# Kernel tuning notes

Measured on AMD Instinct MI355X. Metric: run time of the kernel, lower is better.

The kernel has to match this reference:

```python
import jax, jax.numpy as jnp
import numpy as np

EMB = 1024
HEADS = 16
B, N = 2, 2048

def setup_inputs() -> dict:
    key = jax.random.key(0)
    ks = jax.random.split(key, 9)
    s = 1.0 / np.sqrt(EMB)
    return {
        "x": jax.random.normal(ks[0], (B, N, EMB), dtype=jnp.float32),
        "Wq": jax.random.normal(ks[1], (EMB, EMB), dtype=jnp.float32) * s,
        "bq": jax.random.normal(ks[2], (EMB,), dtype=jnp.float32) * 0.01,
        "Wk": jax.random.normal(ks[3], (EMB, EMB), dtype=jnp.float32) * s,
        "bk": jax.random.normal(ks[4], (EMB,), dtype=jnp.float32) * 0.01,
        "Wv": jax.random.normal(ks[5], (EMB, EMB), dtype=jnp.float32) * s,
        "bv": jax.random.normal(ks[6], (EMB,), dtype=jnp.float32) * 0.01,
        "Wo": jax.random.normal(ks[7], (EMB, EMB), dtype=jnp.float32) * s,
        "bo": jax.random.normal(ks[8], (EMB,), dtype=jnp.float32) * 0.01,
    }

def _split_heads(t):
    b, n, e = t.shape
    return t.reshape(b, n, HEADS, e // HEADS).transpose(0, 2, 1, 3)  # b h n d

def reference(x, Wq, bq, Wk, bk, Wv, bv, Wo, bo):
    q = _split_heads(x @ Wq + bq)
    k = _split_heads(x @ Wk + bk)
    v = _split_heads(x @ Wv + bv)
    # NOTE: original scales by sqrt(emb_size), not sqrt(head_dim)
    scaling = jnp.asarray(EMB, x.dtype) ** 0.5
    energy = jnp.einsum('bhqd,bhkd->bhqk', q, k)
    att = jax.nn.softmax(energy / scaling, axis=-1)
    out = jnp.einsum('bhqk,bhkd->bhqd', att, v)
    out = out.transpose(0, 2, 1, 3).reshape(x.shape[0], x.shape[1], EMB)
    return out @ Wo + bo
```

## Files before the change

kernel.cpp:

```cpp
#include <hip/hip_runtime.h>
#include <hip/hip_bf16.h>

typedef __bf16 bf16_t;
typedef bf16_t bf16x8 __attribute__((ext_vector_type(8)));
typedef float f32x4 __attribute__((ext_vector_type(4)));
typedef float f32x2 __attribute__((ext_vector_type(2)));
typedef float f32x16 __attribute__((ext_vector_type(16)));

#define EMB 1024
#define HEADS 16
#define BATCH 2
#define SEQ 2048
#define HD 64
#define TOKENS (BATCH * SEQ)

__device__ __forceinline__ void gld16(bf16_t* lds_dst, const bf16_t* g_src) {
    __builtin_amdgcn_global_load_lds(
        (const __attribute__((address_space(1))) unsigned int*)g_src,
        (__attribute__((address_space(3))) unsigned int*)lds_dst, 16, 0, 0);
}

__device__ __forceinline__ unsigned cvt_pk_bf16(float lo, float hi) {
    unsigned r;
    asm("v_cvt_pk_bf16_f32 %0, %1, %2" : "=v"(r) : "v"(lo), "v"(hi));
    return r;
}

__device__ __forceinline__ float exp2_fast(float x) {
#if __has_builtin(__builtin_amdgcn_exp2f)
    return __builtin_amdgcn_exp2f(x);
#else
    return __expf(x * 0.69314718056f);
#endif
}

#define WAITV(N) asm volatile("s_waitcnt vmcnt(" #N ")" ::: "memory")
#define BAR() __builtin_amdgcn_s_barrier()

__global__ __launch_bounds__(256) void prep_all(
    const float* __restrict__ x, bf16_t* __restrict__ xb,
    const float* __restrict__ W0, const float* __restrict__ W1,
    const float* __restrict__ W2, const float* __restrict__ W3,
    bf16_t* __restrict__ T0, bf16_t* __restrict__ T1,
    bf16_t* __restrict__ T2, bf16_t* __restrict__ T3) {
    __shared__ __align__(16) bf16_t T[64][72];
    if (blockIdx.x < 1024) {
        size_t i = ((size_t)blockIdx.x * 256 + threadIdx.x) * 16;
        f32x4 v0 = *(const f32x4*)&x[i];
        f32x4 v1 = *(const f32x4*)&x[i + 4];
        f32x4 v2 = *(const f32x4*)&x[i + 8];
        f32x4 v3 = *(const f32x4*)&x[i + 12];
        bf16x8 o0, o1;
#pragma unroll
        for (int j = 0; j < 4; ++j) {
            o0[j] = (bf16_t)v0[j]; o0[4 + j] = (bf16_t)v1[j];
            o1[j] = (bf16_t)v2[j]; o1[4 + j] = (bf16_t)v3[j];
        }
        *(bf16x8*)&xb[i] = o0;
        *(bf16x8*)&xb[i + 8] = o1;
        return;
    }
    int t = blockIdx.x - 1024;
    int z = t >> 8, rid = t & 255;
    const float* src = (z == 0) ? W0 : (z == 1) ? W1 : (z == 2) ? W2 : W3;
    bf16_t* dst = (z == 0) ? T0 : (z == 1) ? T1 : (z == 2) ? T2 : T3;
    int k0 = (rid >> 4) * 64, n0 = (rid & 15) * 64;
    int r = threadIdx.x >> 2, c4 = (threadIdx.x & 3) * 16;
    f32x4 v[4];
#pragma unroll
    for (int q = 0; q < 4; ++q)
        v[q] = *(const f32x4*)&src[(size_t)(k0 + r) * 1024 + n0 + c4 + q * 4];
#pragma unroll
    for (int j = 0; j < 16; ++j) T[c4 + j][r] = (bf16_t)v[j >> 2][j & 3];
    __syncthreads();
    bf16x8 o0 = *(const bf16x8*)&T[r][c4];
    bf16x8 o1 = *(const bf16x8*)&T[r][c4 + 8];
    *(bf16x8*)&dst[(size_t)(n0 + r) * 1024 + k0 + c4] = o0;
    *(bf16x8*)&dst[(size_t)(n0 + r) * 1024 + k0 + c4 + 8] = o1;
}

template <typename TO>
__global__ __launch_bounds__(512) void gemm256(
    const bf16_t* __restrict__ A, const bf16_t* __restrict__ W,
    const float* __restrict__ b0, const float* __restrict__ b1, const float* __restrict__ b2,
    TO* __restrict__ o0, TO* __restrict__ o1, TO* __restrict__ o2,
    int md0, int md1, int md2, float sc0, float sc1, float sc2,
    int MP, int CM, int CSH, int NP) {
    __shared__ __align__(16) bf16_t As[3][256 * 64];
    __shared__ __align__(16) bf16_t Bs[3][128 * 64];

    const int tid = threadIdx.x, w = tid >> 6, lane = tid & 63;
    const int quad = lane >> 4, c = lane & 15;
    const int wm = (w >> 1) * 64, wn = (w & 1) * 64;

    const int lin = blockIdx.x;
    const int xc = lin & 7, t = lin >> 3;
    const int mi = MP * (xc & CM) + (t % MP);
    const int ni = NP * (xc >> CSH) + (t / MP);
    const int m0 = mi * 256, n0 = ni * 128;

    const int z = n0 >> 10;
    const float* bias = (z == 0) ? b0 : (z == 1) ? b1 : b2;
    TO* out = (z == 0) ? o0 : (z == 1) ? o1 : o2;
    const int mode = (z == 0) ? md0 : (z == 1) ? md1 : md2;
    const float scale = (z == 0) ? sc0 : (z == 1) ? sc1 : sc2;
    const int nz = n0 & 1023;

    f32x4 acc[4][4];
#pragma unroll
    for (int i = 0; i < 4; ++i)
#pragma unroll
        for (int j = 0; j < 4; ++j) acc[i][j] = (f32x4){0.f, 0.f, 0.f, 0.f};

    const int r8 = lane >> 3, sg = lane & 7;
    const int g8 = (sg ^ r8) * 8;
    const bf16_t* Ag = A + (size_t)m0 * 1024;
    const bf16_t* Bg = W + (size_t)n0 * 1024;
    int gA[4], lA[4], gB[2], lB[2];
#pragma unroll
    for (int s = 0; s < 4; ++s) {
        lA[s] = (w * 32 + s * 8) * 64;
        gA[s] = (w * 32 + s * 8 + r8) * 1024 + g8;
    }
#pragma unroll
    for (int s = 0; s < 2; ++s) {
        lB[s] = (w * 16 + s * 8) * 64;
        gB[s] = (w * 16 + s * 8 + r8) * 1024 + g8;
    }

    const int so = (quad ^ (c & 7)) * 8;
    int rA[4], rB[4];
#pragma unroll
    for (int i = 0; i < 4; ++i) {
        rA[i] = (wm + i * 16 + c) * 64;
        rB[i] = (wn + i * 16 + c) * 64;
    }

#define STAGE(BUF, T)                                                          \
    {                                                                          \
        int kn = (T) * 64;                                                     \
        _Pragma("unroll")                                                      \
        for (int s = 0; s < 4; ++s) gld16(&As[BUF][lA[s]], &Ag[gA[s] + kn]);   \
        _Pragma("unroll")                                                      \
        for (int s = 0; s < 2; ++s) gld16(&Bs[BUF][lB[s]], &Bg[gB[s] + kn]);   \
    }

#define FRAGS(CUR)                                                             \
    {                                                                          \
        _Pragma("unroll")                                                      \
        for (int ks = 0; ks < 2; ++ks) {                                       \
            int sk = so ^ (ks << 5);                                           \
            bf16x8 af[4], bfv[4];                                              \
            _Pragma("unroll")                                                  \
            for (int i = 0; i < 4; ++i)                                        \
                af[i] = *(const bf16x8*)&As[CUR][rA[i] + sk];                  \
            _Pragma("unroll")                                                  \
            for (int i = 0; i < 4; ++i)                                        \
                bfv[i] = *(const bf16x8*)&Bs[CUR][rB[i] + sk];                 \
            __builtin_amdgcn_s_setprio(1);                                     \
            _Pragma("unroll")                                                  \
            for (int mt = 0; mt < 4; ++mt)                                     \
                _Pragma("unroll")                                              \
                for (int nt = 0; nt < 4; ++nt)                                 \
                    acc[mt][nt] = __builtin_amdgcn_mfma_f32_16x16x32_bf16(     \
                        af[mt], bfv[nt], acc[mt][nt], 0, 0, 0);                \
            __builtin_amdgcn_s_setprio(0);                                     \
        }                                                                      \
    }

#define GSTEP(T, CUR)                                                          \
    {                                                                          \
        WAITV(6);                                                              \
        BAR();                                                                 \
        STAGE(((CUR) + 2) % 3, (T) + 2)                                        \
        FRAGS(CUR)                                                             \
    }

    STAGE(0, 0)
    STAGE(1, 1)
    for (int T = 0; T < 12; T += 3) {
        GSTEP(T, 0)
        GSTEP(T + 1, 1)
        GSTEP(T + 2, 2)
    }
    GSTEP(12, 0)
    GSTEP(13, 1)
    WAITV(6); BAR(); FRAGS(2)
    WAITV(0); BAR(); FRAGS(0)
#undef GSTEP
#undef FRAGS
#undef STAGE

    typedef TO TOx4 __attribute__((ext_vector_type(4)));
#pragma unroll
    for (int nt = 0; nt < 4; ++nt) {
        int colz = nz + wn + nt * 16 + c;
        float bv = bias[colz];
#pragma unroll
        for (int mt = 0; mt < 4; ++mt) {
            if (mode == 2) {
                int row = m0 + wm + mt * 16 + quad * 4;
                int bb = row >> 11, n = row & 2047;
                int hh = colz >> 6, d = colz & 63;
                TOx4 pk;
#pragma unroll
                for (int r = 0; r < 4; ++r)
                    pk[r] = (TO)((acc[mt][nt][r] + bv) * scale);
                *(TOx4*)&out[((size_t)(bb * HEADS + hh) * HD + d) * SEQ + n] = pk;
            } else {
#pragma unroll
                for (int r = 0; r < 4; ++r) {
                    int row = m0 + wm + mt * 16 + quad * 4 + r;
                    float v = (acc[mt][nt][r] + bv) * scale;
                    size_t idx;
                    if (mode == 0) {
                        idx = (size_t)row * 1024 + colz;
                    } else {
                        int bb = row >> 11, n = row & 2047;
                        int hh = colz >> 6, d = colz & 63;
                        idx = ((size_t)(bb * HEADS + hh) * SEQ + n) * HD + d;
                    }
                    out[idx] = (TO)v;
                }
            }
        }
    }
}

__global__ __launch_bounds__(256, 2) void attn_kernel(
    const bf16_t* __restrict__ Q, const bf16_t* __restrict__ K,
    const bf16_t* __restrict__ Vt, bf16_t* __restrict__ O) {
    __shared__ __align__(16) bf16_t Ks[2][2 * 64 * 64];
    __shared__ __align__(16) bf16_t Vs[2][2 * 64 * 64];

    const int tid = threadIdx.x, w = tid >> 6, lane = tid & 63;
    const int hi = lane >> 5, lq = lane & 31;

    const int lin = blockIdx.x + (blockIdx.y << 4);
    const int xcd = lin & 7, slot = lin >> 3;
    const int bh = xcd + ((slot >> 4) << 3);
    const int q0 = (slot & 15) << 7;
    const int b = bh >> 4, h = bh & 15;

    const int srow8 = lane >> 3, sch = lane & 7;

    const bf16_t* Kg0 = K + (size_t)bh * SEQ * HD;
    const bf16_t* Vg0 = Vt + (size_t)bh * HD * SEQ;

    int sl[2], sgK[2], sgV[2];
#pragma unroll
    for (int s = 0; s < 2; ++s) {
        int rg = (w * 2 + s) * 8;
        int row = rg + srow8;
        int g = sch ^ (row & 7);
        sl[s] = rg * 64;
        sgK[s] = row * 64 + g * 8;
        sgV[s] = row * SEQ + g * 8;
    }
    int rd[4];
#pragma unroll
    for (int dc = 0; dc < 4; ++dc)
        rd[dc] = lq * 64 + (((dc * 2 + hi) ^ (lq & 7)) * 8);

    bf16x8 qf[4];
    {
        const bf16_t* Qrow = Q + ((size_t)bh * SEQ + q0 + w * 32 + lq) * HD;
#pragma unroll
        for (int dc = 0; dc < 4; ++dc)
            qf[dc] = *(const bf16x8*)&Qrow[(dc * 2 + hi) * 8];
    }

#define STAGEPH(BUF, PH)                                                       \
    {                                                                          \
        const bf16_t* Kp = Kg0 + (size_t)(PH) * 128 * HD;                      \
        const bf16_t* Vp = Vg0 + (PH) * 128;                                   \
        _Pragma("unroll")                                                      \
        for (int s = 0; s < 2; ++s) {                                          \
            gld16(&Ks[BUF][sl[s]], &Kp[sgK[s]]);                               \
            gld16(&Ks[BUF][4096 + sl[s]], &Kp[4096 + sgK[s]]);                 \
            gld16(&Vs[BUF][sl[s]], &Vp[sgV[s]]);                               \
            gld16(&Vs[BUF][4096 + sl[s]], &Vp[64 + sgV[s]]);                   \
        }                                                                      \
    }

    STAGEPH(0, 0)

    f32x16 Zf;
#pragma unroll
    for (int r = 0; r < 16; ++r) Zf[r] = 0.f;

    f32x16 Oacc0, Oacc1;
#pragma unroll
    for (int r = 0; r < 16; ++r) { Oacc0[r] = 0.f; Oacc1[r] = 0.f; }
    f32x2 lpA = (f32x2){0.f, 0.f}, lpB = (f32x2){0.f, 0.f};

#define PACKFRAG(SS, c2, dstIdx)                                               \
        {                                                                      \
            unsigned pa = cvt_pk_bf16(SS[8 * (c2) + 0], SS[8 * (c2) + 1]);     \
            unsigned pb = cvt_pk_bf16(SS[8 * (c2) + 4], SS[8 * (c2) + 5]);     \
            unsigned pc = cvt_pk_bf16(SS[8 * (c2) + 2], SS[8 * (c2) + 3]);     \
            unsigned pd = cvt_pk_bf16(SS[8 * (c2) + 6], SS[8 * (c2) + 7]);     \
            asm volatile("v_permlane32_swap_b32 %0, %1" : "+v"(pa), "+v"(pb)); \
            asm volatile("v_permlane32_swap_b32 %0, %1" : "+v"(pc), "+v"(pd)); \
            union { unsigned u[4]; bf16x8 v; } pu;                             \
            pu.u[0] = pa; pu.u[1] = pc; pu.u[2] = pb; pu.u[3] = pd;            \
            pf[dstIdx] = pu.v;                                                 \
        }

#define MFMA32(A, B, C) __builtin_amdgcn_mfma_f32_32x32x16_bf16(A, B, C, 0, 0, 0)

#define ACORE2(BUF)                                                            \
    {                                                                          \
        f32x16 SA0, SA1, SB0, SB1;                                             \
        __builtin_amdgcn_s_setprio(1);                                         \
        {                                                                      \
            bf16x8 a0 = *(const bf16x8*)&Ks[BUF][rd[0]];                       \
            bf16x8 a1 = *(const bf16x8*)&Ks[BUF][rd[0] + 2048];                \
            bf16x8 b0 = *(const bf16x8*)&Ks[BUF][rd[0] + 4096];                \
            bf16x8 b1 = *(const bf16x8*)&Ks[BUF][rd[0] + 6144];                \
            SA0 = MFMA32(a0, qf[0], Zf);                                       \
            SA1 = MFMA32(a1, qf[0], Zf);                                       \
            SB0 = MFMA32(b0, qf[0], Zf);                                       \
            SB1 = MFMA32(b1, qf[0], Zf);                                       \
        }                                                                      \
        _Pragma("unroll")                                                      \
        for (int dc = 1; dc < 4; ++dc) {                                       \
            bf16x8 a0 = *(const bf16x8*)&Ks[BUF][rd[dc]];                      \
            bf16x8 a1 = *(const bf16x8*)&Ks[BUF][rd[dc] + 2048];               \
            bf16x8 b0 = *(const bf16x8*)&Ks[BUF][rd[dc] + 4096];               \
            bf16x8 b1 = *(const bf16x8*)&Ks[BUF][rd[dc] + 6144];               \
            SA0 = MFMA32(a0, qf[dc], SA0);                                     \
            SA1 = MFMA32(a1, qf[dc], SA1);                                     \
            SB0 = MFMA32(b0, qf[dc], SB0);                                     \
            SB1 = MFMA32(b1, qf[dc], SB1);                                     \
        }                                                                      \
        __builtin_amdgcn_s_setprio(0);                                         \
        _Pragma("unroll")                                                      \
        for (int r = 0; r < 16; r += 2) {                                      \
            SA0[r] = exp2_fast(SA0[r]); SA0[r + 1] = exp2_fast(SA0[r + 1]);    \
            lpA += (f32x2){SA0[r], SA0[r + 1]};                                \
            SA1[r] = exp2_fast(SA1[r]); SA1[r + 1] = exp2_fast(SA1[r + 1]);    \
            lpB += (f32x2){SA1[r], SA1[r + 1]};                                \
            SB0[r] = exp2_fast(SB0[r]); SB0[r + 1] = exp2_fast(SB0[r + 1]);    \
            lpA += (f32x2){SB0[r], SB0[r + 1]};                                \
            SB1[r] = exp2_fast(SB1[r]); SB1[r + 1] = exp2_fast(SB1[r + 1]);    \
            lpB += (f32x2){SB1[r], SB1[r + 1]};                                \
        }                                                                      \
        bf16x8 pf[8];                                                          \
        PACKFRAG(SA0, 0, 0) PACKFRAG(SA0, 1, 1)                                \
        PACKFRAG(SA1, 0, 2) PACKFRAG(SA1, 1, 3)                                \
        PACKFRAG(SB0, 0, 4) PACKFRAG(SB0, 1, 5)                                \
        PACKFRAG(SB1, 0, 6) PACKFRAG(SB1, 1, 7)                                \
        __builtin_amdgcn_s_setprio(1);                                         \
        _Pragma("unroll")                                                      \
        for (int f = 0; f < 4; ++f) {                                          \
            bf16x8 vA0 = *(const bf16x8*)&Vs[BUF][rd[f]];                      \
            bf16x8 vA1 = *(const bf16x8*)&Vs[BUF][rd[f] + 2048];               \
            bf16x8 vB0 = *(const bf16x8*)&Vs[BUF][rd[f] + 4096];               \
            bf16x8 vB1 = *(const bf16x8*)&Vs[BUF][rd[f] + 6144];               \
            Oacc0 = MFMA32(pf[f], vA0, Oacc0);                                 \
            Oacc1 = MFMA32(pf[f], vA1, Oacc1);                                 \
            Oacc0 = MFMA32(pf[4 + f], vB0, Oacc0);                             \
            Oacc1 = MFMA32(pf[4 + f], vB1, Oacc1);                             \
        }                                                                      \
        __builtin_amdgcn_s_setprio(0);                                         \
    }

    for (int p = 0; p < 16; p += 2) {
        WAITV(0);
        BAR();
        STAGEPH(1, p + 1)
        ACORE2(0)
        WAITV(0);
        BAR();
        if (p < 14) STAGEPH(0, p + 2)
        ACORE2(1)
    }
#undef ACORE2
#undef MFMA32
#undef PACKFRAG
#undef STAGEPH

    float lp = (lpA[0] + lpA[1]) + (lpB[0] + lpB[1]);
    lp += __shfl_xor(lp, 32);
    float rl = 1.0f / lp;

#pragma unroll
    for (int r = 0; r < 16; ++r) {
        int q_loc = (r & 3) + 8 * (r >> 2) + 4 * hi;
        float rr = __shfl(rl, q_loc);
        int qrow = q0 + w * 32 + q_loc;
        size_t base = ((size_t)(b * SEQ + qrow)) * EMB + h * 64;
        O[base + lq] = (bf16_t)(Oacc0[r] * rr);
        O[base + 32 + lq] = (bf16_t)(Oacc1[r] * rr);
    }
}

extern "C" void kernel_launch(void* const* d_in, const int* in_sizes, int n_in,
                              void* d_out, int out_size, void* d_ws, size_t ws_size,
                              hipStream_t stream) {
    (void)in_sizes; (void)n_in; (void)out_size; (void)ws_size;
    const float* x  = (const float*)d_in[0];
    const float* Wq = (const float*)d_in[1];
    const float* bq = (const float*)d_in[2];
    const float* Wk = (const float*)d_in[3];
    const float* bk = (const float*)d_in[4];
    const float* Wv = (const float*)d_in[5];
    const float* bv = (const float*)d_in[6];
    const float* Wo = (const float*)d_in[7];
    const float* bo = (const float*)d_in[8];

    bf16_t* ws = (bf16_t*)d_ws;
    const size_t NELEM = (size_t)TOKENS * EMB;
    const size_t WELEM = (size_t)EMB * EMB;
    bf16_t* Qb  = ws;
    bf16_t* Kb  = ws + NELEM;
    bf16_t* Vtb = ws + 2 * NELEM;
    bf16_t* Ob  = ws + 3 * NELEM;
    bf16_t* xb  = ws + 4 * NELEM;
    bf16_t* Wt0 = ws + 5 * NELEM;
    bf16_t* Wt1 = Wt0 + WELEM;
    bf16_t* Wt2 = Wt0 + 2 * WELEM;
    bf16_t* Wt3 = Wt0 + 3 * WELEM;
    (void)Wt1; (void)Wt2;

    hipLaunchKernelGGL(prep_all, dim3(2048), dim3(256), 0, stream,
                       x, xb, Wq, Wk, Wv, Wo, Wt0, Wt1, Wt2, Wt3);
    hipLaunchKernelGGL((gemm256<bf16_t>), dim3(384), dim3(512), 0, stream,
                       xb, Wt0, bq, bk, bv, Qb, Kb, Vtb,
                       1, 1, 2, 0.0450842204f, 1.0f, 1.0f,
                       4, 3, 2, 12);
    hipLaunchKernelGGL(attn_kernel, dim3(16, 32), dim3(256), 0, stream, Qb, Kb, Vtb, Ob);
    hipLaunchKernelGGL((gemm256<float>), dim3(128), dim3(512), 0, stream,
                       Ob, Wt3, bo, bo, bo,
                       (float*)d_out, (float*)d_out, (float*)d_out,
                       0, 0, 0, 1.0f, 1.0f, 1.0f,
                       2, 7, 3, 8);
}
```

Measured before the change: 198.0 us.

## Add 256x256-tile 8-phase pipelined GEMM for fused QKV projection

Introduces a new GEMM kernel with 256x256 output tiles, double-buffered LDS, and an 8-phase schedule. Each phase interleaves LDS fragment reads, async global-to-LDS loads of the next tile halves, and MFMA bursts at raised priority. The QKV projection switches to it with half as many workgroups, aiming for more reuse per loaded byte and better overlap of loads with math. The cost is a larger accumulator register footprint, more barriers, and fewer blocks (192) to fill the GPU's compute units.

```diff
diff --git a/kernel.cpp b/kernel.cpp
--- a/kernel.cpp
+++ b/kernel.cpp
@@ -35,6 +35,7 @@
 }
 
 #define WAITV(N) asm volatile("s_waitcnt vmcnt(" #N ")" ::: "memory")
+#define WAITLGKM() asm volatile("s_waitcnt lgkmcnt(0)" ::: "memory")
 #define BAR() __builtin_amdgcn_s_barrier()
 
 __global__ __launch_bounds__(256) void prep_all(
@@ -77,6 +78,170 @@
     bf16x8 o1 = *(const bf16x8*)&T[r][c4 + 8];
     *(bf16x8*)&dst[(size_t)(n0 + r) * 1024 + k0 + c4] = o0;
     *(bf16x8*)&dst[(size_t)(n0 + r) * 1024 + k0 + c4 + 8] = o1;
+}
+
+template <typename TO>
+__global__ __launch_bounds__(512) void gemm8p(
+    const bf16_t* __restrict__ A, const bf16_t* __restrict__ W,
+    const float* __restrict__ b0, const float* __restrict__ b1, const float* __restrict__ b2,
+    TO* __restrict__ o0, TO* __restrict__ o1, TO* __restrict__ o2,
+    int md0, int md1, int md2, float sc0, float sc1, float sc2,
+    int XMP, int XNP, int CXM, int CXS) {
+    __shared__ __align__(16) bf16_t As[2][256 * 64];
+    __shared__ __align__(16) bf16_t Bs[2][256 * 64];
+
+    const int tid = threadIdx.x, w = tid >> 6, lane = tid & 63;
+    const int quad = lane >> 4, cc = lane & 15;
+    const int wr = w >> 2, wc = w & 3;
+
+    const int lin = blockIdx.x;
+    const int xc = lin & 7, t = lin >> 3;
+    const int mi = (xc & CXM) * XMP + (t % XMP);
+    const int ni = (xc >> CXS) * XNP + (t / XMP);
+    const int m0 = mi * 256, n0 = ni * 256;
+
+    const int z = n0 >> 10;
+    const float* bias = (z == 0) ? b0 : (z == 1) ? b1 : b2;
+    TO* out = (z == 0) ? o0 : (z == 1) ? o1 : o2;
+    const int mode = (z == 0) ? md0 : (z == 1) ? md1 : md2;
+    const float scale = (z == 0) ? sc0 : (z == 1) ? sc1 : sc2;
+    const int nz = n0 & 1023;
+
+    f32x4 acc[8][4];
+#pragma unroll
+    for (int i = 0; i < 8; ++i)
+#pragma unroll
+        for (int j = 0; j < 4; ++j) acc[i][j] = (f32x4){0.f, 0.f, 0.f, 0.f};
+
+    const int r8 = lane >> 3, sg = lane & 7;
+    const int g8 = (sg ^ r8) * 8;
+    const bf16_t* Ag = A + (size_t)m0 * 1024;
+    const bf16_t* Bg = W + (size_t)n0 * 1024;
+
+#define ST_A(BUF, TILE, H)                                                     \
+    {                                                                          \
+        _Pragma("unroll")                                                      \
+        for (int s = 0; s < 2; ++s) {                                          \
+            int rg = (H) * 128 + (w * 2 + s) * 8;                              \
+            gld16(&As[BUF][rg * 64],                                           \
+                  &Ag[(size_t)(rg + r8) * 1024 + (TILE) * 64 + g8]);           \
+        }                                                                      \
+    }
+#define ST_B(BUF, TILE, H)                                                     \
+    {                                                                          \
+        _Pragma("unroll")                                                      \
+        for (int s = 0; s < 2; ++s) {                                          \
+            int rg = (H) * 128 + (w * 2 + s) * 8;                              \
+            gld16(&Bs[BUF][rg * 64],                                           \
+                  &Bg[(size_t)(rg + r8) * 1024 + (TILE) * 64 + g8]);           \
+        }                                                                      \
+    }
+
+    const int soq = (quad ^ (cc & 7)) * 8;
+    int rArow[8], rBrow[4];
+#pragma unroll
+    for (int mt = 0; mt < 8; ++mt) rArow[mt] = (wr * 128 + mt * 16 + cc) * 64;
+#pragma unroll
+    for (int nt = 0; nt < 4; ++nt) rBrow[nt] = (wc * 64 + nt * 16 + cc) * 64;
+
+    bf16x8 bfr[4][2];
+#define RD_B(BUF)                                                              \
+    {                                                                          \
+        _Pragma("unroll")                                                      \
+        for (int nt = 0; nt < 4; ++nt) {                                       \
+            bfr[nt][0] = *(const bf16x8*)&Bs[BUF][rBrow[nt] + soq];            \
+            bfr[nt][1] = *(const bf16x8*)&Bs[BUF][rBrow[nt] + (soq ^ 32)];     \
+        }                                                                      \
+    }
+
+#define PHASE(BUF, Q, STG)                                                     \
+    {                                                                          \
+        bf16x8 af0a = *(const bf16x8*)&As[BUF][rArow[(Q) * 2] + soq];          \
+        bf16x8 af0b = *(const bf16x8*)&As[BUF][rArow[(Q) * 2] + (soq ^ 32)];   \
+        bf16x8 af1a = *(const bf16x8*)&As[BUF][rArow[(Q) * 2 + 1] + soq];      \
+        bf16x8 af1b = *(const bf16x8*)&As[BUF][rArow[(Q) * 2 + 1] + (soq ^ 32)]; \
+        STG;                                                                   \
+        WAITLGKM();                                                            \
+        __builtin_amdgcn_sched_barrier(0);                                     \
+        __builtin_amdgcn_s_setprio(1);                                         \
+        _Pragma("unroll")                                                      \
+        for (int nt = 0; nt < 4; ++nt) {                                       \
+            acc[(Q) * 2][nt] = __builtin_amdgcn_mfma_f32_16x16x32_bf16(        \
+                af0a, bfr[nt][0], acc[(Q) * 2][nt], 0, 0, 0);                  \
+            acc[(Q) * 2][nt] = __builtin_amdgcn_mfma_f32_16x16x32_bf16(        \
+                af0b, bfr[nt][1], acc[(Q) * 2][nt], 0, 0, 0);                  \
+            acc[(Q) * 2 + 1][nt] = __builtin_amdgcn_mfma_f32_16x16x32_bf16(    \
+                af1a, bfr[nt][0], acc[(Q) * 2 + 1][nt], 0, 0, 0);              \
+            acc[(Q) * 2 + 1][nt] = __builtin_amdgcn_mfma_f32_16x16x32_bf16(    \
+                af1b, bfr[nt][1], acc[(Q) * 2 + 1][nt], 0, 0, 0);              \
+        }                                                                      \
+        __builtin_amdgcn_s_setprio(0);                                         \
+    }
+
+    ST_A(0, 0, 0) ST_A(0, 0, 1) ST_B(0, 0, 0) ST_B(0, 0, 1)
+    ST_B(1, 1, 0) ST_B(1, 1, 1)
+
+    for (int i = 0; i < 8; ++i) {
+        WAITV(4);
+        BAR();
+        RD_B(0)
+        PHASE(0, 0, ST_A(1, 2 * i + 1, 0))
+        BAR();
+        PHASE(0, 1, ST_A(1, 2 * i + 1, 1))
+        BAR();
+        PHASE(0, 2, if (i < 7) ST_B(0, 2 * i + 2, 0))
+        BAR();
+        PHASE(0, 3, if (i < 7) ST_B(0, 2 * i + 2, 1))
+        if (i < 7) { WAITV(4); } else { WAITV(0); }
+        BAR();
+        RD_B(1)
+        PHASE(1, 0, if (i < 7) ST_A(0, 2 * i + 2, 0))
+        BAR();
+        PHASE(1, 1, if (i < 7) ST_A(0, 2 * i + 2, 1))
+        BAR();
+        PHASE(1, 2, if (i < 7) ST_B(1, 2 * i + 3, 0))
+        BAR();
+        PHASE(1, 3, if (i < 7) ST_B(1, 2 * i + 3, 1))
+    }
+#undef PHASE
+#undef RD_B
+#undef ST_A
+#undef ST_B
+
+    typedef TO TOx4 __attribute__((ext_vector_type(4)));
+#pragma unroll
+    for (int nt = 0; nt < 4; ++nt) {
+        int colz = nz + wc * 64 + nt * 16 + cc;
+        float bv = bias[colz];
+#pragma unroll
+        for (int mt = 0; mt < 8; ++mt) {
+            if (mode == 2) {
+                int row = m0 + wr * 128 + mt * 16 + quad * 4;
+                int bb = row >> 11, n = row & 2047;
+                int hh = colz >> 6, d = colz & 63;
+                TOx4 pk;
+#pragma unroll
+                for (int r = 0; r < 4; ++r)
+                    pk[r] = (TO)((acc[mt][nt][r] + bv) * scale);
+                *(TOx4*)&out[((size_t)(bb * HEADS + hh) * HD + d) * SEQ + n] = pk;
+            } else {
+#pragma unroll
+                for (int r = 0; r < 4; ++r) {
+                    int row = m0 + wr * 128 + mt * 16 + quad * 4 + r;
+                    float v = (acc[mt][nt][r] + bv) * scale;
+                    size_t idx;
+                    if (mode == 0) {
+                        idx = (size_t)row * 1024 + colz;
+                    } else {
+                        int bb = row >> 11, n = row & 2047;
+                        int hh = colz >> 6, d = colz & 63;
+                        idx = ((size_t)(bb * HEADS + hh) * SEQ + n) * HD + d;
+                    }
+                    out[idx] = (TO)v;
+                }
+            }
+        }
+    }
 }
 
 template <typename TO>
@@ -426,10 +591,10 @@
 
     hipLaunchKernelGGL(prep_all, dim3(2048), dim3(256), 0, stream,
                        x, xb, Wq, Wk, Wv, Wo, Wt0, Wt1, Wt2, Wt3);
-    hipLaunchKernelGGL((gemm256<bf16_t>), dim3(384), dim3(512), 0, stream,
+    hipLaunchKernelGGL((gemm8p<bf16_t>), dim3(192), dim3(512), 0, stream,
                        xb, Wt0, bq, bk, bv, Qb, Kb, Vtb,
                        1, 1, 2, 0.0450842204f, 1.0f, 1.0f,
-                       4, 3, 2, 12);
+                       4, 6, 3, 2);
     hipLaunchKernelGGL(attn_kernel, dim3(16, 32), dim3(256), 0, stream, Qb, Kb, Vtb, Ob);
     hipLaunchKernelGGL((gemm256<float>), dim3(128), dim3(512), 0, stream,
                        Ob, Wt3, bo, bo, bo,
```

New measurement: 190.9 us, median of 2. 1.04x faster.
